# Kernel tuning notes

Hardware: AMD Instinct MI355X
Metric: run time of the kernel (lower is better)

Reference implementation:

```python
import jax, jax.numpy as jnp
import numpy as np

B, T, V, H, L = 2048, 128, 256, 20, 15  # batch, seq_len, vocab, hidden, max_label


def setup_inputs() -> dict:
    key = jax.random.key(0)
    ks = jax.random.split(key, 8)
    g = lambda k, shape, s: (jax.random.normal(k, shape, jnp.float32) * s)
    return {
        "x": jax.random.randint(ks[0], (B, T), 0, V, dtype=jnp.int32),
        "W0": g(ks[1], (V, 3 * H), 0.06),   # input kernel layer 0 [V, 3H] (z|r|h)
        "U0": g(ks[2], (H, 3 * H), 0.2),    # recurrent kernel layer 0
        "b0i": jnp.zeros((3 * H,), jnp.float32),  # input bias (reset_after=True split bias)
        "b0r": jnp.zeros((3 * H,), jnp.float32),  # recurrent bias
        "W1": g(ks[3], (H, 3 * H), 0.2),
        "U1": g(ks[4], (H, 3 * H), 0.2),
        "b1i": jnp.zeros((3 * H,), jnp.float32),
        "b1r": jnp.zeros((3 * H,), jnp.float32),
        "Wd": g(ks[5], (H, L), 0.2),
        "bd": jnp.zeros((L,), jnp.float32),
        "drop_rate": 0,  # identity dropout (deterministic reference)
    }


def _gru_cell(h, xw, U, br):
    # Keras GRUCell with reset_after=True:
    #   xw = x @ W + b_in  (precomputed), rec = h @ U + b_rec
    rec = h @ U + br
    xz, xr, xh = jnp.split(xw, 3, axis=-1)
    rz, rr, rh = jnp.split(rec, 3, axis=-1)
    z = jax.nn.sigmoid(xz + rz)
    r = jax.nn.sigmoid(xr + rr)
    hh = jnp.tanh(xh + r * rh)
    return z * h + (1.0 - z) * hh


def reference(x, W0, U0, b0i, b0r, W1, U1, b1i, b1r, Wd, bd, drop_rate):
    # one_hot(x) @ W0 == gather rows of W0 (same math, no [B,T,V] materialization)
    xW0 = W0[x] + b0i                 # [B, T, 3H]
    xW0 = jnp.swapaxes(xW0, 0, 1)     # [T, B, 3H] for scan over time

    def step(carry, xw_t):
        h0, h1 = carry
        h0 = _gru_cell(h0, xw_t, U0, b0r)
        xw1 = h0 @ W1 + b1i
        h1 = _gru_cell(h1, xw1, U1, b1r)
        return (h0, h1), None

    h0 = jnp.zeros((x.shape[0], H), W0.dtype)
    h1 = jnp.zeros((x.shape[0], H), W0.dtype)
    (h0, h1), _ = jax.lax.scan(step, (h0, h1), xW0)
    # tf.nn.dropout with rate 0 is the identity
    out = h1
    logits = jax.nn.softmax(out @ Wd + bd, axis=-1)  # [B, L]
    return logits
```

## Files before the change

### kernel.cpp

```cpp
#include <hip/hip_runtime.h>


#define BB 2048
#define TT 128
#define HH 20
#define LL 15
#define H3 60

__device__ __forceinline__ float bclane(float v, int k) {
    return __int_as_float(__builtin_amdgcn_readlane(__float_as_int(v), k));
}
__device__ __forceinline__ float bperm(int byteaddr, float v) {
    return __int_as_float(__builtin_amdgcn_ds_bpermute(byteaddr, __float_as_int(v)));
}
__device__ __forceinline__ float fast_rcp(float x) { return __builtin_amdgcn_rcpf(x); }
__device__ __forceinline__ float sigm(float x) { return fast_rcp(1.f + __expf(-x)); }
__device__ __forceinline__ float tanh_f(float x) { return 1.f - 2.f * fast_rcp(1.f + __expf(2.f * x)); }
#define PIN(v) asm volatile("" : "+v"(v))

extern "C" __global__ __launch_bounds__(256)
__attribute__((amdgpu_waves_per_eu(2, 2)))
void gru2_kernel(const int* __restrict__ x, const float* __restrict__ W0,
                 const float* __restrict__ U0, const float* __restrict__ b0i,
                 const float* __restrict__ b0r, const float* __restrict__ W1,
                 const float* __restrict__ U1, const float* __restrict__ b1i,
                 const float* __restrict__ b1r, const float* __restrict__ Wd,
                 const float* __restrict__ bd, float* __restrict__ out)
{
    const int lane = threadIdx.x & 63;
    const int b = blockIdx.x * 4 + (threadIdx.x >> 6);
    const int c = lane < H3 ? lane : H3 - 1;

    float u0c[HH], w1c[HH], u1c[HH];
#pragma unroll
    for (int k = 0; k < HH; ++k) {
        u0c[k] = U0[k * H3 + c];
        w1c[k] = W1[k * H3 + c];
        u1c[k] = U1[k * H3 + c];
    }
#pragma unroll
    for (int k = 0; k < HH; ++k) { PIN(u0c[k]); PIN(w1c[k]); PIN(u1c[k]); }
    float bi0 = b0i[c], br0 = b0r[c], bi1 = b1i[c], br1 = b1r[c];
    PIN(bi0); PIN(br0); PIN(bi1); PIN(br1);

    const int* xrow = x + b * TT;
    const int tokA = xrow[lane];
    const int tokB = xrow[64 + lane];

    const int aR = ((lane - 20) & 63) << 2;
    const int aZ = ((lane - 40) & 63) << 2;

    float h0 = 0.f, h1 = 0.f;

    const int tok0 = __builtin_amdgcn_readlane(tokA, 0);
    const int tok1 = __builtin_amdgcn_readlane(tokA, 1);
    int tokn2 = __builtin_amdgcn_readlane(tokA, 2);
    float xw_cur = W0[tok0 * H3 + c] + bi0;
    float xw_nxt = W0[tok1 * H3 + c];

#pragma unroll 2
    for (int t = 0; t < TT; ++t) {
        const int t3 = (t + 3 < TT) ? (t + 3) : (TT - 1);
        const float xw_pf = W0[tokn2 * H3 + c];
        const int tokn3 = __builtin_amdgcn_readlane(t3 < 64 ? tokA : tokB, t3 & 63);

        float hb0[HH];
#pragma unroll
        for (int k = 0; k < HH; ++k) hb0[k] = bclane(h0, 40 + k);
        float a0 = br0, a1 = 0.f;
#pragma unroll
        for (int k = 0; k < 10; ++k) a0 = fmaf(hb0[k], u0c[k], a0);
#pragma unroll
        for (int k = 10; k < HH; ++k) a1 = fmaf(hb0[k], u0c[k], a1);
        const float rec0 = a0 + a1;

        const float sg0 = sigm(xw_cur + rec0);
        const float rv0 = bperm(aR, sg0);
        const float zv0 = bperm(aZ, sg0);
        const float hh0 = tanh_f(xw_cur + rv0 * rec0);
        h0 = fmaf(zv0, h0 - hh0, hh0);

        float hc0[HH], hc1[HH];
#pragma unroll
        for (int k = 0; k < HH; ++k) { hc0[k] = bclane(h0, 40 + k); hc1[k] = bclane(h1, 40 + k); }
        float xa = bi1, xb = 0.f, ra = br1, rb = 0.f;
#pragma unroll
        for (int k = 0; k < 10; ++k) {
            xa = fmaf(hc0[k], w1c[k], xa);
            ra = fmaf(hc1[k], u1c[k], ra);
        }
#pragma unroll
        for (int k = 10; k < HH; ++k) {
            xb = fmaf(hc0[k], w1c[k], xb);
            rb = fmaf(hc1[k], u1c[k], rb);
        }
        const float xw1 = xa + xb, rec1 = ra + rb;

        const float sg1 = sigm(xw1 + rec1);
        const float rv1 = bperm(aR, sg1);
        const float zv1 = bperm(aZ, sg1);
        const float hh1 = tanh_f(xw1 + rv1 * rec1);
        h1 = fmaf(zv1, h1 - hh1, hh1);

        xw_cur = xw_nxt + bi0;
        xw_nxt = xw_pf;
        tokn2 = tokn3;
    }

    const int l = lane < LL ? lane : LL - 1;
    float acc = bd[l];
#pragma unroll
    for (int k = 0; k < HH; ++k)
        acc = fmaf(bclane(h1, 40 + k), Wd[k * LL + l], acc);

    float m = acc;
#pragma unroll
    for (int i = 0; i < LL; ++i) m = fmaxf(m, bclane(acc, i));
    const float e = __expf(acc - m);
    float s = 0.f;
#pragma unroll
    for (int i = 0; i < LL; ++i) s += bclane(e, i);
    const float p = e * fast_rcp(s);

    if (lane < LL) out[b * LL + lane] = p;
}

extern "C" void kernel_launch(void* const* d_in, const int* in_sizes, int n_in,
                              void* d_out, int out_size, void* d_ws, size_t ws_size,
                              hipStream_t stream) {
    const int*   x   = (const int*)  d_in[0];
    const float* W0  = (const float*)d_in[1];
    const float* U0  = (const float*)d_in[2];
    const float* b0i = (const float*)d_in[3];
    const float* b0r = (const float*)d_in[4];
    const float* W1  = (const float*)d_in[5];
    const float* U1  = (const float*)d_in[6];
    const float* b1i = (const float*)d_in[7];
    const float* b1r = (const float*)d_in[8];
    const float* Wd  = (const float*)d_in[9];
    const float* bd  = (const float*)d_in[10];
    float* out = (float*)d_out;

    dim3 grid(BB / 4), block(256);
    hipLaunchKernelGGL(gru2_kernel, grid, block, 0, stream,
                       x, W0, U0, b0i, b0r, W1, U1, b1i, b1r, Wd, bd, out);
}
```

Baseline: 148.3 us.

## Broadcast hidden states via LDS float4 reads with packed FMA for recurrent matvecs

Replaces the per-element readlane broadcasts of h0 and h1 for the recurrent matvecs with writes of the hidden state into a per-wave LDS buffer. Every lane then reads it back as float4 vectors and accumulates with packed two-wide FMAs (v2f), with the U0 and U1 columns stored in pairs. The aim is to cut scalar readlane traffic and halve the FMA instruction count. In exchange it adds LDS store-to-load latency on the serial recurrence and depends on implicit wave-level ordering without explicit barriers. The W1 input projection still uses readlane broadcasts.

```diff
diff --git a/kernel.cpp b/kernel.cpp
--- a/kernel.cpp
+++ b/kernel.cpp
@@ -6,6 +6,8 @@
 #define HH 20
 #define LL 15
 #define H3 60
+
+typedef float v2f __attribute__((ext_vector_type(2)));
 
 __device__ __forceinline__ float bclane(float v, int k) {
     return __int_as_float(__builtin_amdgcn_readlane(__float_as_int(v), k));
@@ -28,18 +30,28 @@
                  const float* __restrict__ bd, float* __restrict__ out)
 {
     const int lane = threadIdx.x & 63;
-    const int b = blockIdx.x * 4 + (threadIdx.x >> 6);
+    const int w = threadIdx.x >> 6;
+    const int b = blockIdx.x * 4 + w;
     const int c = lane < H3 ? lane : H3 - 1;
 
-    float u0c[HH], w1c[HH], u1c[HH];
+    __shared__ __align__(16) float hbuf[4][2][24];
+    float* h0buf = &hbuf[w][0][0];
+    float* h1buf = &hbuf[w][1][0];
+    if (lane >= 40 && lane < H3) { h0buf[lane - 40] = 0.f; h1buf[lane - 40] = 0.f; }
+
+    v2f u0p[HH / 2], u1p[HH / 2];
+    float w1c[HH];
 #pragma unroll
-    for (int k = 0; k < HH; ++k) {
-        u0c[k] = U0[k * H3 + c];
-        w1c[k] = W1[k * H3 + c];
-        u1c[k] = U1[k * H3 + c];
+    for (int p = 0; p < HH / 2; ++p) {
+        u0p[p] = v2f{U0[(2 * p) * H3 + c], U0[(2 * p + 1) * H3 + c]};
+        u1p[p] = v2f{U1[(2 * p) * H3 + c], U1[(2 * p + 1) * H3 + c]};
     }
 #pragma unroll
-    for (int k = 0; k < HH; ++k) { PIN(u0c[k]); PIN(w1c[k]); PIN(u1c[k]); }
+    for (int k = 0; k < HH; ++k) w1c[k] = W1[k * H3 + c];
+#pragma unroll
+    for (int p = 0; p < HH / 2; ++p) { PIN(u0p[p]); PIN(u1p[p]); }
+#pragma unroll
+    for (int k = 0; k < HH; ++k) PIN(w1c[k]);
     float bi0 = b0i[c], br0 = b0r[c], bi1 = b1i[c], br1 = b1r[c];
     PIN(bi0); PIN(br0); PIN(bi1); PIN(br1);
 
@@ -64,15 +76,15 @@
         const float xw_pf = W0[tokn2 * H3 + c];
         const int tokn3 = __builtin_amdgcn_readlane(t3 < 64 ? tokA : tokB, t3 & 63);
 
-        float hb0[HH];
+        const float4* h0q = (const float4*)h0buf;
+        v2f a0 = v2f{br0, 0.f};
 #pragma unroll
-        for (int k = 0; k < HH; ++k) hb0[k] = bclane(h0, 40 + k);
-        float a0 = br0, a1 = 0.f;
-#pragma unroll
-        for (int k = 0; k < 10; ++k) a0 = fmaf(hb0[k], u0c[k], a0);
-#pragma unroll
-        for (int k = 10; k < HH; ++k) a1 = fmaf(hb0[k], u0c[k], a1);
-        const float rec0 = a0 + a1;
+        for (int q = 0; q < 5; ++q) {
+            const float4 hv = h0q[q];
+            a0 = __builtin_elementwise_fma(v2f{hv.x, hv.y}, u0p[2 * q], a0);
+            a0 = __builtin_elementwise_fma(v2f{hv.z, hv.w}, u0p[2 * q + 1], a0);
+        }
+        const float rec0 = a0.x + a0.y;
 
         const float sg0 = sigm(xw_cur + rec0);
         const float rv0 = bperm(aR, sg0);
@@ -80,27 +92,32 @@
         const float hh0 = tanh_f(xw_cur + rv0 * rec0);
         h0 = fmaf(zv0, h0 - hh0, hh0);
 
-        float hc0[HH], hc1[HH];
+        if (lane >= 40 && lane < H3) h0buf[lane - 40] = h0;
+
+        const float4* h1q = (const float4*)h1buf;
+        v2f a1 = v2f{br1, 0.f};
 #pragma unroll
-        for (int k = 0; k < HH; ++k) { hc0[k] = bclane(h0, 40 + k); hc1[k] = bclane(h1, 40 + k); }
-        float xa = bi1, xb = 0.f, ra = br1, rb = 0.f;
+        for (int q = 0; q < 5; ++q) {
+            const float4 hv = h1q[q];
+            a1 = __builtin_elementwise_fma(v2f{hv.x, hv.y}, u1p[2 * q], a1);
+            a1 = __builtin_elementwise_fma(v2f{hv.z, hv.w}, u1p[2 * q + 1], a1);
+        }
+        const float rec1 = a1.x + a1.y;
+
+        float xa = bi1, xb = 0.f;
 #pragma unroll
-        for (int k = 0; k < 10; ++k) {
-            xa = fmaf(hc0[k], w1c[k], xa);
-            ra = fmaf(hc1[k], u1c[k], ra);
-        }
+        for (int k = 0; k < 10; ++k) xa = fmaf(bclane(h0, 40 + k), w1c[k], xa);
 #pragma unroll
-        for (int k = 10; k < HH; ++k) {
-            xb = fmaf(hc0[k], w1c[k], xb);
-            rb = fmaf(hc1[k], u1c[k], rb);
-        }
-        const float xw1 = xa + xb, rec1 = ra + rb;
+        for (int k = 10; k < HH; ++k) xb = fmaf(bclane(h0, 40 + k), w1c[k], xb);
+        const float xw1 = xa + xb;
 
         const float sg1 = sigm(xw1 + rec1);
         const float rv1 = bperm(aR, sg1);
         const float zv1 = bperm(aZ, sg1);
         const float hh1 = tanh_f(xw1 + rv1 * rec1);
         h1 = fmaf(zv1, h1 - hh1, hh1);
+
+        if (lane >= 40 && lane < H3) h1buf[lane - 40] = h1;
 
         xw_cur = xw_nxt + bi0;
         xw_nxt = xw_pf;
```

After: 143.0 us. -3.6%, faster.
